# Kernel optimization log

Measured on AMD Instinct MI355X. Metric: run time of the kernel, lower is better.

Reference implementation:

```python
import jax, jax.numpy as jnp
import numpy as np

ROI_SIZES = (3, 7, 11)
IMAGE_SIZE = 960.0


def setup_inputs() -> dict:
    key = jax.random.key(0)
    ks = jax.random.split(key, 12)
    B, C, H, W = 1, 64, 120, 120
    N = 4096
    feature_maps = jax.random.normal(ks[0], (B, C, H, W), jnp.float32)
    cx = jax.random.uniform(ks[1], (N,), jnp.float32, 100.0, 860.0)
    cy = jax.random.uniform(ks[2], (N,), jnp.float32, 100.0, 860.0)
    bw = jax.random.uniform(ks[3], (N,), jnp.float32, 20.0, 240.0)
    bh = jax.random.uniform(ks[4], (N,), jnp.float32, 20.0, 240.0)
    boxes = jnp.stack([cx - bw / 2, cy - bh / 2, cx + bw / 2, cy + bh / 2], axis=1)
    s = 0.05
    w1 = jax.random.normal(ks[5], (64, 128), jnp.float32) * s
    b1 = jnp.zeros((128,), jnp.float32)
    w2 = jax.random.normal(ks[6], (128, 64), jnp.float32) * s
    b2 = jnp.zeros((64,), jnp.float32)
    p1 = jax.random.normal(ks[7], (256, 128), jnp.float32) * s
    pb1 = jnp.zeros((128,), jnp.float32)
    p2 = jax.random.normal(ks[8], (128, 64), jnp.float32) * s
    pb2 = jnp.zeros((64,), jnp.float32)
    return dict(feature_maps=feature_maps, boxes=boxes, w1=w1, b1=b1, w2=w2, b2=b2,
                p1=p1, pb1=pb1, p2=p2, pb2=pb2)


def _roi_pool(fm0, boxes_norm, r):
    """affine_grid + bilinear grid_sample (align_corners=False, zeros pad) + global avg pool.
    fm0: [C,H,W], boxes_norm: [N,4] in [-1,1]. Returns [N,C]."""
    C, H, W = fm0.shape
    x1, y1, x2, y2 = boxes_norm[:, 0], boxes_norm[:, 1], boxes_norm[:, 2], boxes_norm[:, 3]
    cx = (x1 + x2) / 2
    cy = (y1 + y2) / 2
    bw = jnp.clip(x2 - x1, 1e-6, None)
    bh = jnp.clip(y2 - y1, 1e-6, None)
    # affine_grid base coords with align_corners=False: (2i+1)/r - 1
    lin = (2.0 * jnp.arange(r, dtype=jnp.float32) + 1.0) / r - 1.0
    gx = cx[:, None, None] + (bw / 2)[:, None, None] * lin[None, None, :]  # [N,r,r]
    gy = cy[:, None, None] + (bh / 2)[:, None, None] * lin[None, :, None]  # [N,r,r]
    # normalized -> pixel coords (align_corners=False)
    ix = ((gx + 1.0) * W - 1.0) / 2.0
    iy = ((gy + 1.0) * H - 1.0) / 2.0
    x0f = jnp.floor(ix)
    y0f = jnp.floor(iy)
    wx1 = ix - x0f
    wy1 = iy - y0f
    x0 = x0f.astype(jnp.int32)
    y0 = y0f.astype(jnp.int32)
    fm_flat = fm0.reshape(C, H * W)

    def corner(xi, yi, wt):
        valid = (xi >= 0) & (xi < W) & (yi >= 0) & (yi < H)
        xi_c = jnp.clip(xi, 0, W - 1)
        yi_c = jnp.clip(yi, 0, H - 1)
        idx = yi_c * W + xi_c  # [N,r,r]
        vals = jnp.take(fm_flat, idx.reshape(-1), axis=1).reshape(C, *idx.shape)  # [C,N,r,r]
        return vals * (wt * valid.astype(wt.dtype))[None]

    out = (corner(x0, y0, (1 - wx1) * (1 - wy1))
           + corner(x0 + 1, y0, wx1 * (1 - wy1))
           + corner(x0, y0 + 1, (1 - wx1) * wy1)
           + corner(x0 + 1, y0 + 1, wx1 * wy1))
    return out.mean(axis=(2, 3)).T  # [N,C]


def _shared_head(x, w1, b1, w2, b2):
    h = jax.nn.relu(x @ w1 + b1)
    return jax.nn.relu(h @ w2 + b2)


def reference(feature_maps, boxes, w1, b1, w2, b2, p1, pb1, p2, pb2):
    B, C, H, W = feature_maps.shape
    N = boxes.shape[0]
    boxes_norm = boxes / IMAGE_SIZE * 2.0 - 1.0
    fm0 = feature_maps[0]
    feats = []
    for r in ROI_SIZES:
        pooled = _roi_pool(fm0, boxes_norm, r)  # [N,C]
        feats.append(_shared_head(pooled, w1, b1, w2, b2))
    # global context: avg-pool full map, expand to N
    g = feature_maps.mean(axis=(2, 3))  # [B,C], B=1
    g = jnp.broadcast_to(g, (N, C))
    feats.append(_shared_head(g, w1, b1, w2, b2))
    concat = jnp.concatenate(feats, axis=1)  # [N, 4*64]
    h = jax.nn.relu(concat @ p1 + pb1)
    return jax.nn.relu(h @ p2 + pb2)
```

## Files before the change

### kernel.cpp

```cpp
#include <hip/hip_runtime.h>
#include <hip/hip_bf16.h>


#define HW 120
#define NPIX (HW * HW)

__global__ __launch_bounds__(256) void k_transpose_mean(
    const float* __restrict__ fm, float* __restrict__ fm_t,
    float* __restrict__ partial)
{
    __shared__ float tile[64][65];
    __shared__ float pr[4][64];
    const int t  = threadIdx.x;
    const int tx = t & 63;
    const int ty = t >> 6;
    const int pix0 = blockIdx.x * 64;

    #pragma unroll
    for (int k = 0; k < 16; ++k) {
        const int c = k * 4 + ty;
        tile[c][tx] = fm[c * NPIX + pix0 + tx];
    }
    __syncthreads();
    #pragma unroll
    for (int k = 0; k < 16; ++k) {
        const int p = k * 4 + ty;
        fm_t[(pix0 + p) * 64 + tx] = tile[tx][p];
    }
    float s = 0.f;
    #pragma unroll
    for (int k = 0; k < 16; ++k) s += tile[tx][ty * 16 + k];
    pr[ty][tx] = s;
    __syncthreads();
    if (t < 64)
        partial[blockIdx.x * 64 + t] = pr[0][t] + pr[1][t] + pr[2][t] + pr[3][t];
}

__global__ __launch_bounds__(256) void k_ghead(
    const float* __restrict__ partial,
    const float* __restrict__ w1, const float* __restrict__ b1,
    const float* __restrict__ w2, const float* __restrict__ b2,
    const float* __restrict__ p1, const float* __restrict__ pb1,
    float* __restrict__ f1pre)
{
    __shared__ float pr[4][64];
    __shared__ float g[64];
    __shared__ float h[128];
    __shared__ float gh[64];
    const int t = threadIdx.x;
    const int c = t & 63, q = t >> 6;
    float s = 0.f;
    for (int b = q; b < 225; b += 4) s += partial[b * 64 + c];
    pr[q][c] = s;
    __syncthreads();
    if (t < 64) g[t] = (pr[0][t] + pr[1][t] + pr[2][t] + pr[3][t]) * (1.f / 14400.f);
    __syncthreads();
    if (t < 128) {
        float a = b1[t];
        #pragma unroll 8
        for (int cc = 0; cc < 64; ++cc) a = fmaf(g[cc], w1[cc * 128 + t], a);
        h[t] = fmaxf(a, 0.f);
    }
    __syncthreads();
    if (t < 64) {
        float a = b2[t];
        #pragma unroll 8
        for (int k = 0; k < 128; ++k) a = fmaf(h[k], w2[k * 64 + t], a);
        gh[t] = fmaxf(a, 0.f);
    }
    __syncthreads();
    if (t < 128) {
        float a = pb1[t];
        #pragma unroll 8
        for (int j = 0; j < 64; ++j) a = fmaf(gh[j], p1[(192 + j) * 128 + t], a);
        f1pre[t] = a;
    }
}

template <int R>
__device__ __forceinline__ float4 gather8(
    const char* __restrict__ fb, int g8,
    float cx, float cy, float bw2, float bh2)
{
    constexpr float invR = 1.f / (float)R;
    constexpr float s2   = invR * invR;
    float ax = 0.f, ay = 0.f, az = 0.f, aw = 0.f;
    #pragma unroll 2
    for (int lp = g8; lp < R * R; lp += 8) {
        const int i = lp / R;
        const int j = lp - i * R;
        const float liny = (float)(2 * i + 1) * invR - 1.f;
        const float linx = (float)(2 * j + 1) * invR - 1.f;
        const float gy = cy + bh2 * liny;
        const float gx = cx + bw2 * linx;
        const float iy = ((gy + 1.f) * 120.f - 1.f) * 0.5f;
        const float ix = ((gx + 1.f) * 120.f - 1.f) * 0.5f;
        const float y0f = floorf(iy), x0f = floorf(ix);
        const float wy = iy - y0f,  wx = ix - x0f;
        const int y0 = (int)y0f, x0 = (int)x0f;
        const float vy0 = (y0 >= 0 && y0 < HW)      ? 1.f : 0.f;
        const float vy1 = (y0 >= -1 && y0 < HW - 1) ? 1.f : 0.f;
        const float vx0 = (x0 >= 0 && x0 < HW)      ? 1.f : 0.f;
        const float vx1 = (x0 >= -1 && x0 < HW - 1) ? 1.f : 0.f;
        const int x0c = min(max(x0, 0), HW - 1);
        const int x1c = min(max(x0 + 1, 0), HW - 1);
        const int y0c = min(max(y0, 0), HW - 1);
        const int y1c = min(max(y0 + 1, 0), HW - 1);
        const int o00 = (y0c * HW + x0c) * 256;
        const int o01 = (y0c * HW + x1c) * 256;
        const int o10 = (y1c * HW + x0c) * 256;
        const int o11 = (y1c * HW + x1c) * 256;
        const float w00 = (1.f - wx) * (1.f - wy) * s2 * (vy0 * vx0);
        const float w01 = wx * (1.f - wy) * s2 * (vy0 * vx1);
        const float w10 = (1.f - wx) * wy * s2 * (vy1 * vx0);
        const float w11 = wx * wy * s2 * (vy1 * vx1);
        const float4 v0 = *(const float4*)(fb + o00);
        const float4 v1 = *(const float4*)(fb + o01);
        const float4 v2 = *(const float4*)(fb + o10);
        const float4 v3 = *(const float4*)(fb + o11);
        ax = fmaf(w00, v0.x, ax); ay = fmaf(w00, v0.y, ay);
        az = fmaf(w00, v0.z, az); aw = fmaf(w00, v0.w, aw);
        ax = fmaf(w01, v1.x, ax); ay = fmaf(w01, v1.y, ay);
        az = fmaf(w01, v1.z, az); aw = fmaf(w01, v1.w, aw);
        ax = fmaf(w10, v2.x, ax); ay = fmaf(w10, v2.y, ay);
        az = fmaf(w10, v2.z, az); aw = fmaf(w10, v2.w, aw);
        ax = fmaf(w11, v3.x, ax); ay = fmaf(w11, v3.y, ay);
        az = fmaf(w11, v3.z, az); aw = fmaf(w11, v3.w, aw);
    }
    ax += __shfl_xor(ax, 16, 64); ay += __shfl_xor(ay, 16, 64);
    az += __shfl_xor(az, 16, 64); aw += __shfl_xor(aw, 16, 64);
    ax += __shfl_xor(ax, 32, 64); ay += __shfl_xor(ay, 32, 64);
    az += __shfl_xor(az, 32, 64); aw += __shfl_xor(aw, 32, 64);
    return make_float4(ax, ay, az, aw);
}

__global__ __launch_bounds__(256) void k_fused(
    const float* __restrict__ fm_t, const float* __restrict__ boxes,
    const float* __restrict__ w1, const float* __restrict__ b1,
    const float* __restrict__ w2, const float* __restrict__ b2,
    const float* __restrict__ p1, const float* __restrict__ f1pre,
    const float* __restrict__ p2, const float* __restrict__ pb2,
    float* __restrict__ out, int N)
{
    __shared__ __align__(16) float xpart[2][2][192];
    __shared__ __align__(16) float xbuf[2][192];
    __shared__ __align__(16) float hbuf[2][384];
    __shared__ __align__(16) float cbuf[2][192];
    __shared__ __align__(16) float fbuf[2][128];
    __shared__ __align__(16) float opart[2][2][64];

    const int t    = threadIdx.x;
    const int lane = t & 63;
    const int w    = t >> 6;
    const int n0   = blockIdx.x * 2;

    {
        const int b  = w >> 1;
        const int hf = w & 1;
        const int qc = lane & 15;
        const int pg = lane >> 4;
        const int g8 = hf * 4 + pg;
        const int n  = n0 + b;

        if (n < N) {
            const float4 bx = reinterpret_cast<const float4*>(boxes)[n];
            const float x1 = bx.x / 960.f * 2.f - 1.f;
            const float y1 = bx.y / 960.f * 2.f - 1.f;
            const float x2 = bx.z / 960.f * 2.f - 1.f;
            const float y2 = bx.w / 960.f * 2.f - 1.f;
            const float cx  = (x1 + x2) * 0.5f;
            const float cy  = (y1 + y2) * 0.5f;
            const float bw2 = fmaxf(x2 - x1, 1e-6f) * 0.5f;
            const float bh2 = fmaxf(y2 - y1, 1e-6f) * 0.5f;
            const char* fb = (const char*)fm_t + qc * 16;

            const float4 r0 = gather8<3>(fb, g8, cx, cy, bw2, bh2);
            if (pg == 0) *(float4*)(&xpart[b][hf][4 * qc]) = r0;
            const float4 r1 = gather8<7>(fb, g8, cx, cy, bw2, bh2);
            if (pg == 0) *(float4*)(&xpart[b][hf][64 + 4 * qc]) = r1;
            const float4 r2 = gather8<11>(fb, g8, cx, cy, bw2, bh2);
            if (pg == 0) *(float4*)(&xpart[b][hf][128 + 4 * qc]) = r2;
        } else if (pg == 0) {
            const float4 z = make_float4(0.f, 0.f, 0.f, 0.f);
            *(float4*)(&xpart[b][hf][4 * qc]) = z;
            *(float4*)(&xpart[b][hf][64 + 4 * qc]) = z;
            *(float4*)(&xpart[b][hf][128 + 4 * qc]) = z;
        }
    }
    __syncthreads();

    for (int i = t; i < 384; i += 256) {
        const int b = i / 192, r = i - b * 192;
        xbuf[b][r] = xpart[b][0][r] + xpart[b][1][r];
    }
    __syncthreads();

    {
        const int k  = t & 127;
        const int wp = t >> 7;
        const int G0 = wp,     b0 = G0 / 3, s0 = G0 - 3 * b0;
        const int G1 = wp + 2, b1_ = G1 / 3, s1_ = G1 - 3 * b1_;
        const int G2 = wp + 4, b2_ = G2 / 3, s2_ = G2 - 3 * b2_;
        const float* xb0 = xbuf[b0] + s0 * 64;
        const float* xb1 = xbuf[b1_] + s1_ * 64;
        const float* xb2 = xbuf[b2_] + s2_ * 64;
        const float bias = b1[k];
        float a0 = bias, a1 = bias, a2 = bias;
        #pragma unroll 4
        for (int c4 = 0; c4 < 16; ++c4) {
            const float4 xv0 = *(const float4*)(xb0 + 4 * c4);
            const float4 xv1 = *(const float4*)(xb1 + 4 * c4);
            const float4 xv2 = *(const float4*)(xb2 + 4 * c4);
            #define W1LD(CI) w1[(4 * c4 + CI) * 128 + k]
            { const float wv = W1LD(0);
              a0 = fmaf(xv0.x, wv, a0); a1 = fmaf(xv1.x, wv, a1); a2 = fmaf(xv2.x, wv, a2); }
            { const float wv = W1LD(1);
              a0 = fmaf(xv0.y, wv, a0); a1 = fmaf(xv1.y, wv, a1); a2 = fmaf(xv2.y, wv, a2); }
            { const float wv = W1LD(2);
              a0 = fmaf(xv0.z, wv, a0); a1 = fmaf(xv1.z, wv, a1); a2 = fmaf(xv2.z, wv, a2); }
            { const float wv = W1LD(3);
              a0 = fmaf(xv0.w, wv, a0); a1 = fmaf(xv1.w, wv, a1); a2 = fmaf(xv2.w, wv, a2); }
            #undef W1LD
        }
        hbuf[b0][s0 * 128 + k]   = fmaxf(a0, 0.f);
        hbuf[b1_][s1_ * 128 + k] = fmaxf(a1, 0.f);
        hbuf[b2_][s2_ * 128 + k] = fmaxf(a2, 0.f);
    }
    __syncthreads();

    {
        const int co = lane;
        const float bias = b2[co];
        {
            const int G = t >> 6;
            const int b = G / 3, s = G - 3 * (G / 3);
            const float* hb = hbuf[b] + s * 128;
            float a = bias;
            #pragma unroll 4
            for (int c4 = 0; c4 < 32; ++c4) {
                const float4 hv = *(const float4*)(hb + 4 * c4);
                a = fmaf(hv.x, w2[(4 * c4 + 0) * 64 + co], a);
                a = fmaf(hv.y, w2[(4 * c4 + 1) * 64 + co], a);
                a = fmaf(hv.z, w2[(4 * c4 + 2) * 64 + co], a);
                a = fmaf(hv.w, w2[(4 * c4 + 3) * 64 + co], a);
            }
            cbuf[b][s * 64 + co] = fmaxf(a, 0.f);
        }
        if (t < 128) {
            const int G = 4 + (t >> 6);
            const int b = G / 3, s = G - 3 * (G / 3);
            const float* hb = hbuf[b] + s * 128;
            float a = bias;
            #pragma unroll 4
            for (int c4 = 0; c4 < 32; ++c4) {
                const float4 hv = *(const float4*)(hb + 4 * c4);
                a = fmaf(hv.x, w2[(4 * c4 + 0) * 64 + co], a);
                a = fmaf(hv.y, w2[(4 * c4 + 1) * 64 + co], a);
                a = fmaf(hv.z, w2[(4 * c4 + 2) * 64 + co], a);
                a = fmaf(hv.w, w2[(4 * c4 + 3) * 64 + co], a);
            }
            cbuf[b][s * 64 + co] = fmaxf(a, 0.f);
        }
    }
    __syncthreads();

    {
        const int k = t & 127;
        const int b = t >> 7;
        const float* cb = cbuf[b];
        float a = f1pre[k];
        #pragma unroll 4
        for (int q4 = 0; q4 < 48; ++q4) {
            const float4 cv = *(const float4*)(cb + 4 * q4);
            a = fmaf(cv.x, p1[(4 * q4 + 0) * 128 + k], a);
            a = fmaf(cv.y, p1[(4 * q4 + 1) * 128 + k], a);
            a = fmaf(cv.z, p1[(4 * q4 + 2) * 128 + k], a);
            a = fmaf(cv.w, p1[(4 * q4 + 3) * 128 + k], a);
        }
        fbuf[b][k] = fmaxf(a, 0.f);
    }
    __syncthreads();

    {
        const int co = lane;
        const int bb = (t >> 6) & 1;
        const int kh = t >> 7;
        const float* fbp = fbuf[bb] + kh * 64;
        float a = kh ? 0.f : pb2[co];
        #pragma unroll 4
        for (int j4 = 0; j4 < 16; ++j4) {
            const float4 fv = *(const float4*)(fbp + 4 * j4);
            a = fmaf(fv.x, p2[(kh * 64 + 4 * j4 + 0) * 64 + co], a);
            a = fmaf(fv.y, p2[(kh * 64 + 4 * j4 + 1) * 64 + co], a);
            a = fmaf(fv.z, p2[(kh * 64 + 4 * j4 + 2) * 64 + co], a);
            a = fmaf(fv.w, p2[(kh * 64 + 4 * j4 + 3) * 64 + co], a);
        }
        opart[kh][bb][co] = a;
    }
    __syncthreads();
    if (t < 128) {
        const int co = lane;
        const int bb = t >> 6;
        const int n  = n0 + bb;
        if (n < N)
            out[n * 64 + co] = fmaxf(opart[0][bb][co] + opart[1][bb][co], 0.f);
    }
}

extern "C" void kernel_launch(void* const* d_in, const int* in_sizes, int n_in,
                              void* d_out, int out_size, void* d_ws, size_t ws_size,
                              hipStream_t stream)
{
    const float* fm    = (const float*)d_in[0];
    const float* boxes = (const float*)d_in[1];
    const float* w1    = (const float*)d_in[2];
    const float* b1    = (const float*)d_in[3];
    const float* w2    = (const float*)d_in[4];
    const float* b2    = (const float*)d_in[5];
    const float* p1    = (const float*)d_in[6];
    const float* pb1   = (const float*)d_in[7];
    const float* p2    = (const float*)d_in[8];
    const float* pb2   = (const float*)d_in[9];
    float* out = (float*)d_out;

    const int N = in_sizes[1] / 4;

    float* ws      = (float*)d_ws;
    float* fm_t    = ws;
    float* partial = fm_t + 921600;
    float* f1pre   = partial + 14400;

    k_transpose_mean<<<NPIX / 64, 256, 0, stream>>>(fm, fm_t, partial);
    k_ghead<<<1, 256, 0, stream>>>(partial, w1, b1, w2, b2, p1, pb1, f1pre);
    k_fused<<<(N + 1) / 2, 256, 0, stream>>>(fm_t, boxes, w1, b1, w2, b2,
                                             p1, f1pre, p2, pb2, out, N);
}
```

Measured before the change: 160.4 us.

## Split fused pool+MLP kernel into pooling kernel and 16-ROI batched MLP kernel

The single fused kernel is split in two. The first kernel does only the bilinear ROI pooling and writes the pooled features to workspace. The second kernel runs the MLP chain over 16 ROIs per 512-thread block, and each weight load is reused across up to 12 rows held in register accumulators. This cuts the repeated weight traffic that the old 2-ROI-per-block layout paid. In exchange it adds a global round trip for the pooled features and one more kernel launch.

Result: faster. 156.6 us (-2.4%).

```diff
diff --git a/kernel.cpp b/kernel.cpp
--- a/kernel.cpp
+++ b/kernel.cpp
@@ -134,20 +134,11 @@
     return make_float4(ax, ay, az, aw);
 }
 
-__global__ __launch_bounds__(256) void k_fused(
+__global__ __launch_bounds__(256) void k_pool(
     const float* __restrict__ fm_t, const float* __restrict__ boxes,
-    const float* __restrict__ w1, const float* __restrict__ b1,
-    const float* __restrict__ w2, const float* __restrict__ b2,
-    const float* __restrict__ p1, const float* __restrict__ f1pre,
-    const float* __restrict__ p2, const float* __restrict__ pb2,
-    float* __restrict__ out, int N)
+    float* __restrict__ pooled, int N)
 {
     __shared__ __align__(16) float xpart[2][2][192];
-    __shared__ __align__(16) float xbuf[2][192];
-    __shared__ __align__(16) float hbuf[2][384];
-    __shared__ __align__(16) float cbuf[2][192];
-    __shared__ __align__(16) float fbuf[2][128];
-    __shared__ __align__(16) float opart[2][2][64];
 
     const int t    = threadIdx.x;
     const int lane = t & 63;
@@ -180,130 +171,160 @@
             if (pg == 0) *(float4*)(&xpart[b][hf][64 + 4 * qc]) = r1;
             const float4 r2 = gather8<11>(fb, g8, cx, cy, bw2, bh2);
             if (pg == 0) *(float4*)(&xpart[b][hf][128 + 4 * qc]) = r2;
-        } else if (pg == 0) {
-            const float4 z = make_float4(0.f, 0.f, 0.f, 0.f);
-            *(float4*)(&xpart[b][hf][4 * qc]) = z;
-            *(float4*)(&xpart[b][hf][64 + 4 * qc]) = z;
-            *(float4*)(&xpart[b][hf][128 + 4 * qc]) = z;
         }
     }
     __syncthreads();
 
     for (int i = t; i < 384; i += 256) {
         const int b = i / 192, r = i - b * 192;
-        xbuf[b][r] = xpart[b][0][r] + xpart[b][1][r];
-    }
-    __syncthreads();
-
-    {
-        const int k  = t & 127;
-        const int wp = t >> 7;
-        const int G0 = wp,     b0 = G0 / 3, s0 = G0 - 3 * b0;
-        const int G1 = wp + 2, b1_ = G1 / 3, s1_ = G1 - 3 * b1_;
-        const int G2 = wp + 4, b2_ = G2 / 3, s2_ = G2 - 3 * b2_;
-        const float* xb0 = xbuf[b0] + s0 * 64;
-        const float* xb1 = xbuf[b1_] + s1_ * 64;
-        const float* xb2 = xbuf[b2_] + s2_ * 64;
+        const int n = n0 + b;
+        if (n < N) {
+            const int s = r >> 6, c = r & 63;
+            pooled[(s * N + n) * 64 + c] = xpart[b][0][r] + xpart[b][1][r];
+        }
+    }
+}
+
+__global__ __launch_bounds__(512) void k_mlp(
+    const float* __restrict__ pooled,
+    const float* __restrict__ w1, const float* __restrict__ b1,
+    const float* __restrict__ w2, const float* __restrict__ b2,
+    const float* __restrict__ p1, const float* __restrict__ f1pre,
+    const float* __restrict__ p2, const float* __restrict__ pb2,
+    float* __restrict__ out, int N)
+{
+    __shared__ __align__(16) float xls[48 * 64];
+    __shared__ __align__(16) float hls[48 * 128];
+    __shared__ __align__(16) float cls[16 * 192];
+    __shared__ __align__(16) float fls[16 * 128];
+    __shared__ float f1b[128];
+
+    const int t  = threadIdx.x;
+    const int n0 = blockIdx.x * 16;
+
+    for (int i = t; i < 768; i += 512) {
+        const int f = i * 4;
+        const int P = f >> 6;
+        const int c = f & 63;
+        const int b = P / 3;
+        const int s = P - 3 * b;
+        const int n = n0 + b;
+        float4 v = make_float4(0.f, 0.f, 0.f, 0.f);
+        if (n < N) v = *(const float4*)(pooled + (s * N + n) * 64 + c);
+        *(float4*)(xls + f) = v;
+    }
+    if (t < 128) f1b[t] = f1pre[t];
+    __syncthreads();
+
+    {
+        const int k = t & 127;
+        const int g = t >> 7;
         const float bias = b1[k];
-        float a0 = bias, a1 = bias, a2 = bias;
-        #pragma unroll 4
+        float acc[12];
+        #pragma unroll
+        for (int r = 0; r < 12; ++r) acc[r] = bias;
+        #pragma unroll 2
         for (int c4 = 0; c4 < 16; ++c4) {
-            const float4 xv0 = *(const float4*)(xb0 + 4 * c4);
-            const float4 xv1 = *(const float4*)(xb1 + 4 * c4);
-            const float4 xv2 = *(const float4*)(xb2 + 4 * c4);
-            #define W1LD(CI) w1[(4 * c4 + CI) * 128 + k]
-            { const float wv = W1LD(0);
-              a0 = fmaf(xv0.x, wv, a0); a1 = fmaf(xv1.x, wv, a1); a2 = fmaf(xv2.x, wv, a2); }
-            { const float wv = W1LD(1);
-              a0 = fmaf(xv0.y, wv, a0); a1 = fmaf(xv1.y, wv, a1); a2 = fmaf(xv2.y, wv, a2); }
-            { const float wv = W1LD(2);
-              a0 = fmaf(xv0.z, wv, a0); a1 = fmaf(xv1.z, wv, a1); a2 = fmaf(xv2.z, wv, a2); }
-            { const float wv = W1LD(3);
-              a0 = fmaf(xv0.w, wv, a0); a1 = fmaf(xv1.w, wv, a1); a2 = fmaf(xv2.w, wv, a2); }
-            #undef W1LD
-        }
-        hbuf[b0][s0 * 128 + k]   = fmaxf(a0, 0.f);
-        hbuf[b1_][s1_ * 128 + k] = fmaxf(a1, 0.f);
-        hbuf[b2_][s2_ * 128 + k] = fmaxf(a2, 0.f);
-    }
-    __syncthreads();
-
-    {
-        const int co = lane;
+            const float wv0 = w1[(4 * c4 + 0) * 128 + k];
+            const float wv1 = w1[(4 * c4 + 1) * 128 + k];
+            const float wv2 = w1[(4 * c4 + 2) * 128 + k];
+            const float wv3 = w1[(4 * c4 + 3) * 128 + k];
+            #pragma unroll
+            for (int r = 0; r < 12; ++r) {
+                const float4 xv = *(const float4*)(xls + (g + 4 * r) * 64 + 4 * c4);
+                acc[r] = fmaf(xv.x, wv0, acc[r]);
+                acc[r] = fmaf(xv.y, wv1, acc[r]);
+                acc[r] = fmaf(xv.z, wv2, acc[r]);
+                acc[r] = fmaf(xv.w, wv3, acc[r]);
+            }
+        }
+        #pragma unroll
+        for (int r = 0; r < 12; ++r)
+            hls[(g + 4 * r) * 128 + k] = fmaxf(acc[r], 0.f);
+    }
+    __syncthreads();
+
+    {
+        const int co = t & 63;
+        const int w8 = t >> 6;
         const float bias = b2[co];
-        {
-            const int G = t >> 6;
-            const int b = G / 3, s = G - 3 * (G / 3);
-            const float* hb = hbuf[b] + s * 128;
-            float a = bias;
-            #pragma unroll 4
-            for (int c4 = 0; c4 < 32; ++c4) {
-                const float4 hv = *(const float4*)(hb + 4 * c4);
-                a = fmaf(hv.x, w2[(4 * c4 + 0) * 64 + co], a);
-                a = fmaf(hv.y, w2[(4 * c4 + 1) * 64 + co], a);
-                a = fmaf(hv.z, w2[(4 * c4 + 2) * 64 + co], a);
-                a = fmaf(hv.w, w2[(4 * c4 + 3) * 64 + co], a);
+        float acc[6];
+        #pragma unroll
+        for (int r = 0; r < 6; ++r) acc[r] = bias;
+        #pragma unroll 2
+        for (int c4 = 0; c4 < 32; ++c4) {
+            const float wv0 = w2[(4 * c4 + 0) * 64 + co];
+            const float wv1 = w2[(4 * c4 + 1) * 64 + co];
+            const float wv2 = w2[(4 * c4 + 2) * 64 + co];
+            const float wv3 = w2[(4 * c4 + 3) * 64 + co];
+            #pragma unroll
+            for (int r = 0; r < 6; ++r) {
+                const float4 hv = *(const float4*)(hls + (w8 + 8 * r) * 128 + 4 * c4);
+                acc[r] = fmaf(hv.x, wv0, acc[r]);
+                acc[r] = fmaf(hv.y, wv1, acc[r]);
+                acc[r] = fmaf(hv.z, wv2, acc[r]);
+                acc[r] = fmaf(hv.w, wv3, acc[r]);
             }
-            cbuf[b][s * 64 + co] = fmaxf(a, 0.f);
-        }
-        if (t < 128) {
-            const int G = 4 + (t >> 6);
-            const int b = G / 3, s = G - 3 * (G / 3);
-            const float* hb = hbuf[b] + s * 128;
-            float a = bias;
-            #pragma unroll 4
-            for (int c4 = 0; c4 < 32; ++c4) {
-                const float4 hv = *(const float4*)(hb + 4 * c4);
-                a = fmaf(hv.x, w2[(4 * c4 + 0) * 64 + co], a);
-                a = fmaf(hv.y, w2[(4 * c4 + 1) * 64 + co], a);
-                a = fmaf(hv.z, w2[(4 * c4 + 2) * 64 + co], a);
-                a = fmaf(hv.w, w2[(4 * c4 + 3) * 64 + co], a);
+        }
+        #pragma unroll
+        for (int r = 0; r < 6; ++r) {
+            const int P = w8 + 8 * r;
+            const int b = P / 3;
+            const int s = P - 3 * b;
+            cls[b * 192 + s * 64 + co] = fmaxf(acc[r], 0.f);
+        }
+    }
+    __syncthreads();
+
+    {
+        const int k = t & 127;
+        const int g = t >> 7;
+        const float bias = f1b[k];
+        float acc[4];
+        #pragma unroll
+        for (int r = 0; r < 4; ++r) acc[r] = bias;
+        #pragma unroll 2
+        for (int q4 = 0; q4 < 48; ++q4) {
+            const float wv0 = p1[(4 * q4 + 0) * 128 + k];
+            const float wv1 = p1[(4 * q4 + 1) * 128 + k];
+            const float wv2 = p1[(4 * q4 + 2) * 128 + k];
+            const float wv3 = p1[(4 * q4 + 3) * 128 + k];
+            #pragma unroll
+            for (int r = 0; r < 4; ++r) {
+                const float4 cv = *(const float4*)(cls + (g + 4 * r) * 192 + 4 * q4);
+                acc[r] = fmaf(cv.x, wv0, acc[r]);
+                acc[r] = fmaf(cv.y, wv1, acc[r]);
+                acc[r] = fmaf(cv.z, wv2, acc[r]);
+                acc[r] = fmaf(cv.w, wv3, acc[r]);
             }
-            cbuf[b][s * 64 + co] = fmaxf(a, 0.f);
-        }
-    }
-    __syncthreads();
-
-    {
-        const int k = t & 127;
-        const int b = t >> 7;
-        const float* cb = cbuf[b];
-        float a = f1pre[k];
-        #pragma unroll 4
-        for (int q4 = 0; q4 < 48; ++q4) {
-            const float4 cv = *(const float4*)(cb + 4 * q4);
-            a = fmaf(cv.x, p1[(4 * q4 + 0) * 128 + k], a);
-            a = fmaf(cv.y, p1[(4 * q4 + 1) * 128 + k], a);
-            a = fmaf(cv.z, p1[(4 * q4 + 2) * 128 + k], a);
-            a = fmaf(cv.w, p1[(4 * q4 + 3) * 128 + k], a);
-        }
-        fbuf[b][k] = fmaxf(a, 0.f);
-    }
-    __syncthreads();
-
-    {
-        const int co = lane;
-        const int bb = (t >> 6) & 1;
-        const int kh = t >> 7;
-        const float* fbp = fbuf[bb] + kh * 64;
-        float a = kh ? 0.f : pb2[co];
-        #pragma unroll 4
-        for (int j4 = 0; j4 < 16; ++j4) {
-            const float4 fv = *(const float4*)(fbp + 4 * j4);
-            a = fmaf(fv.x, p2[(kh * 64 + 4 * j4 + 0) * 64 + co], a);
-            a = fmaf(fv.y, p2[(kh * 64 + 4 * j4 + 1) * 64 + co], a);
-            a = fmaf(fv.z, p2[(kh * 64 + 4 * j4 + 2) * 64 + co], a);
-            a = fmaf(fv.w, p2[(kh * 64 + 4 * j4 + 3) * 64 + co], a);
-        }
-        opart[kh][bb][co] = a;
-    }
-    __syncthreads();
-    if (t < 128) {
-        const int co = lane;
-        const int bb = t >> 6;
-        const int n  = n0 + bb;
-        if (n < N)
-            out[n * 64 + co] = fmaxf(opart[0][bb][co] + opart[1][bb][co], 0.f);
+        }
+        #pragma unroll
+        for (int r = 0; r < 4; ++r)
+            fls[(g + 4 * r) * 128 + k] = fmaxf(acc[r], 0.f);
+    }
+    __syncthreads();
+
+    {
+        const int co = t & 63;
+        const int w8 = t >> 6;
+        float a0 = pb2[co], a1 = a0;
+        #pragma unroll 2
+        for (int j4 = 0; j4 < 32; ++j4) {
+            const float wv0 = p2[(4 * j4 + 0) * 64 + co];
+            const float wv1 = p2[(4 * j4 + 1) * 64 + co];
+            const float wv2 = p2[(4 * j4 + 2) * 64 + co];
+            const float wv3 = p2[(4 * j4 + 3) * 64 + co];
+            const float4 f0 = *(const float4*)(fls + w8 * 128 + 4 * j4);
+            const float4 f1v = *(const float4*)(fls + (w8 + 8) * 128 + 4 * j4);
+            a0 = fmaf(f0.x, wv0, a0);  a1 = fmaf(f1v.x, wv0, a1);
+            a0 = fmaf(f0.y, wv1, a0);  a1 = fmaf(f1v.y, wv1, a1);
+            a0 = fmaf(f0.z, wv2, a0);  a1 = fmaf(f1v.z, wv2, a1);
+            a0 = fmaf(f0.w, wv3, a0);  a1 = fmaf(f1v.w, wv3, a1);
+        }
+        const int na = n0 + w8;
+        const int nb = n0 + w8 + 8;
+        if (na < N) out[na * 64 + co] = fmaxf(a0, 0.f);
+        if (nb < N) out[nb * 64 + co] = fmaxf(a1, 0.f);
     }
 }
 
@@ -329,9 +350,11 @@
     float* fm_t    = ws;
     float* partial = fm_t + 921600;
     float* f1pre   = partial + 14400;
+    float* pooled  = f1pre + 128;
 
     k_transpose_mean<<<NPIX / 64, 256, 0, stream>>>(fm, fm_t, partial);
     k_ghead<<<1, 256, 0, stream>>>(partial, w1, b1, w2, b2, p1, pb1, f1pre);
-    k_fused<<<(N + 1) / 2, 256, 0, stream>>>(fm_t, boxes, w1, b1, w2, b2,
+    k_pool<<<(N + 1) / 2, 256, 0, stream>>>(fm_t, boxes, pooled, N);
+    k_mlp<<<(N + 15) / 16, 512, 0, stream>>>(pooled, w1, b1, w2, b2,
                                              p1, f1pre, p2, pb2, out, N);
 }
```
